# Kernel optimization log

Measured on AMD Instinct MI355X. Metric: run time of the kernel, lower is better.

Reference implementation:

```python
import jax, jax.numpy as jnp
import numpy as np

NUM_NEIGHBORS = (10, 25)  # FLAGS.num_neighbors = '10_25'
MAX_DEGREE = 64
L = 2  # num encoder layers


def _sample(nodes, neighbors_out, neighbors_in, key):
    """Multi-hop uniform neighbor sampling (shuffle columns + slice, as in TF code)."""
    samples = [nodes]
    support = 1
    supports = [1]
    for k in range(L):
        t = L - 1 - k
        n = NUM_NEIGHBORS[t]
        support *= 2 * n
        supports.append(support)
        key, k1, k2 = jax.random.split(key, 3)
        # tf.transpose(tf.random.shuffle(tf.transpose(x))) shuffles neighbor slots
        # with ONE permutation shared across all rows, then slices first n.
        cols_out = jax.random.permutation(k1, MAX_DEGREE)[:n]
        cols_in = jax.random.permutation(k2, MAX_DEGREE)[:n]
        nout = neighbors_out[samples[k]][:, cols_out]  # [prev, n]
        nin = neighbors_in[samples[k]][:, cols_in]     # [prev, n]
        samples.append(jnp.concatenate([nout, nin], axis=1).reshape(-1))
    return samples, supports


def _gc(self_v, nei_out, nei_in, W):
    # GraphConvolution: mean-aggregate out/in neighbors, concat with self, linear, sigmoid.
    agg = jnp.concatenate([self_v, nei_out.mean(axis=1), nei_in.mean(axis=1)], axis=-1)
    return jax.nn.sigmoid(agg @ W)


def _aggregate(inputs, supports, layer, W, B):
    h_hop = []
    for hop in range(L - layer):
        n = NUM_NEIGHBORS[L - hop - 1]
        nei = inputs[hop + 1].reshape(B * supports[hop], 2 * n, -1)
        self_v = inputs[hop].reshape(B * supports[hop], -1)
        h_hop.append(_gc(self_v, nei[:, :n], nei[:, n:], W))
    return h_hop


def _forward(nodes1, nodes2, neighbors_out, neighbors_in, features,
             W_in, W_mean, W_std, W_pi, W_ag, W_ad, Wd_mean, Wd_std, Wd_pi):
    B = nodes1.shape[0]
    key = jax.random.key(42)
    k1, k2 = jax.random.split(key)
    s1, sup1 = _sample(nodes1, neighbors_out, neighbors_in, k1)
    s2, sup2 = _sample(nodes2, neighbors_out, neighbors_in, k2)
    in1 = [features[s] for s in s1]  # hop-wise gathered features
    in2 = [features[s] for s in s2]
    # layer 0: shared input GC
    h1 = _aggregate(in1, sup1, 0, W_in, B)
    h2 = _aggregate(in2, sup2, 0, W_in, B)
    # layer 1: parameter heads (mean/std/pi/alpha)
    h_mean1 = _aggregate(h1, sup1, 1, W_mean, B)[0]
    h_mean2 = _aggregate(h2, sup2, 1, W_mean, B)[0]
    h_std1 = _aggregate(h1, sup1, 1, W_std, B)[0]
    h_std2 = _aggregate(h2, sup2, 1, W_std, B)[0]
    h_pi1 = _aggregate(h1, sup1, 1, W_pi, B)[0]
    h_pi2 = _aggregate(h2, sup2, 1, W_pi, B)[0]
    # final fully-connected projections (act = identity)
    z_mean1 = h_mean1 @ Wd_mean
    z_mean2 = h_mean2 @ Wd_mean
    z_std1 = h_std1 @ Wd_std
    z_std2 = h_std2 @ Wd_std
    pi_logit1 = h_pi1 @ Wd_pi
    pi_logit2 = h_pi2 @ Wd_pi
    return jnp.stack([z_mean1, z_std1, pi_logit1, z_mean2, z_std2, pi_logit2])


def setup_inputs() -> dict:
    key = jax.random.key(0)
    ks = jax.random.split(key, 16)
    N, F, B = 200000, 128, 256
    E, D = 128, 64
    inp = {
        'nodes1': jax.random.randint(ks[0], (B,), 0, N, dtype=jnp.int32),
        'nodes2': jax.random.randint(ks[1], (B,), 0, N, dtype=jnp.int32),
        'neighbors_out': jax.random.randint(ks[2], (N, MAX_DEGREE), 0, N, dtype=jnp.int32),
        'neighbors_in': jax.random.randint(ks[3], (N, MAX_DEGREE), 0, N, dtype=jnp.int32),
        'features': jax.random.normal(ks[4], (N, F), dtype=jnp.float32),
        'W_in': jax.random.normal(ks[5], (3 * F, E), dtype=jnp.float32) * 0.05,
        'W_mean': jax.random.normal(ks[6], (3 * E, E), dtype=jnp.float32) * 0.05,
        'W_std': jax.random.normal(ks[7], (3 * E, E), dtype=jnp.float32) * 0.05,
        'W_pi': jax.random.normal(ks[8], (3 * E, E), dtype=jnp.float32) * 0.05,
        'W_ag': jax.random.normal(ks[9], (3 * E, E), dtype=jnp.float32) * 0.05,
        'W_ad': jax.random.normal(ks[10], (3 * E, E), dtype=jnp.float32) * 0.05,
        'Wd_mean': jax.random.normal(ks[11], (E, D), dtype=jnp.float32) * 0.05,
        'Wd_std': jax.random.normal(ks[12], (E, D), dtype=jnp.float32) * 0.05,
        'Wd_pi': jax.random.normal(ks[13], (E, D), dtype=jnp.float32) * 0.05,
    }
    return inp


def reference(nodes1, nodes2, neighbors_out, neighbors_in, features,
              W_in, W_mean, W_std, W_pi, W_ag, W_ad, Wd_mean, Wd_std, Wd_pi):
    return _forward(nodes1, nodes2, neighbors_out, neighbors_in, features,
                    W_in, W_mean, W_std, W_pi, W_ag, W_ad, Wd_mean, Wd_std, Wd_pi)
```

## Files before the change

### kernel.cpp

```cpp
#include <hip/hip_runtime.h>
#include <stdint.h>
#include <math.h>

#define FDIM 128
#define KDIM 384
#define NROWS 26112

struct Cols { int o25[25]; int i25[25]; int o10[10]; int i10[10]; };
struct ColsBoth { Cols c[2]; };

static inline uint32_t rotl32(uint32_t x, uint32_t r){ return (x<<r)|(x>>(32u-r)); }

static void tf2x32(uint32_t k0, uint32_t k1, uint32_t c0, uint32_t c1,
                   uint32_t& o0, uint32_t& o1){
  const uint32_t ra[4] = {13u,15u,26u,6u};
  const uint32_t rb[4] = {17u,29u,16u,24u};
  uint32_t ks2 = k0 ^ k1 ^ 0x1BD11BDAu;
  uint32_t x0 = c0 + k0, x1 = c1 + k1;
  for(int i=0;i<4;i++){ x0 += x1; x1 = rotl32(x1, ra[i]); x1 ^= x0; }
  x0 += k1; x1 += ks2 + 1u;
  for(int i=0;i<4;i++){ x0 += x1; x1 = rotl32(x1, rb[i]); x1 ^= x0; }
  x0 += ks2; x1 += k0 + 2u;
  for(int i=0;i<4;i++){ x0 += x1; x1 = rotl32(x1, ra[i]); x1 ^= x0; }
  x0 += k0; x1 += k1 + 3u;
  for(int i=0;i<4;i++){ x0 += x1; x1 = rotl32(x1, rb[i]); x1 ^= x0; }
  x0 += k1; x1 += ks2 + 4u;
  for(int i=0;i<4;i++){ x0 += x1; x1 = rotl32(x1, ra[i]); x1 ^= x0; }
  x0 += ks2; x1 += k0 + 5u;
  o0 = x0; o1 = x1;
}

static void jax_split_child(uint32_t ka, uint32_t kb, uint32_t i,
                            uint32_t& oa, uint32_t& ob){
  tf2x32(ka, kb, 0u, i, oa, ob);
}

static uint32_t jax_bits32(uint32_t ka, uint32_t kb, uint32_t i){
  uint32_t a,b; tf2x32(ka, kb, 0u, i, a, b);
  return a ^ b;
}

static void jax_perm64(uint32_t ka, uint32_t kb, int* perm){
  uint32_t sa, sb; jax_split_child(ka, kb, 1u, sa, sb);
  uint32_t b[64]; int v[64];
  for(int i=0;i<64;i++){ b[i]=jax_bits32(sa, sb, (uint32_t)i); v[i]=i; }
  for(int i=1;i<64;i++){
    uint32_t bb=b[i]; int vv=v[i]; int j=i-1;
    while(j>=0 && b[j]>bb){ b[j+1]=b[j]; v[j+1]=v[j]; j--; }
    b[j+1]=bb; v[j+1]=vv;
  }
  for(int i=0;i<64;i++) perm[i]=v[i];
}

static void compute_cols(ColsBoth& cb){
  uint32_t k1a,k1b,k2a,k2b;
  jax_split_child(0u, 42u, 0u, k1a, k1b);
  jax_split_child(0u, 42u, 1u, k2a, k2b);
  for(int side=0; side<2; side++){
    uint32_t ka = side ? k2a : k1a;
    uint32_t kb = side ? k2b : k1b;
    uint32_t nka,nkb, c1a,c1b, c2a,c2b;
    jax_split_child(ka,kb,0u,nka,nkb);
    jax_split_child(ka,kb,1u,c1a,c1b);
    jax_split_child(ka,kb,2u,c2a,c2b);
    int p[64];
    jax_perm64(c1a,c1b,p); for(int i=0;i<25;i++) cb.c[side].o25[i]=p[i];
    jax_perm64(c2a,c2b,p); for(int i=0;i<25;i++) cb.c[side].i25[i]=p[i];
    uint32_t d1a,d1b,d2a,d2b;
    jax_split_child(nka,nkb,1u,d1a,d1b);
    jax_split_child(nka,nkb,2u,d2a,d2b);
    jax_perm64(d1a,d1b,p); for(int i=0;i<10;i++) cb.c[side].o10[i]=p[i];
    jax_perm64(d2a,d2b,p); for(int i=0;i<10;i++) cb.c[side].i10[i]=p[i];
  }
}

__device__ __forceinline__ float getc(const float4& v, int i){
  return (i==0)?v.x:(i==1)?v.y:(i==2)?v.z:v.w;
}
__device__ __forceinline__ float sigf(float x){ return 1.0f/(1.0f+expf(-x)); }
__device__ __forceinline__ void add4(float4& s, const float4& v){
  s.x+=v.x; s.y+=v.y; s.z+=v.z; s.w+=v.w;
}
__device__ __forceinline__ void add2(float2& s, const float2& v){
  s.x+=v.x; s.y+=v.y;
}


__global__ __launch_bounds__(256) void gather_kernel(
    const float* __restrict__ feat,
    const int* __restrict__ nodes1, const int* __restrict__ nodes2,
    const int* __restrict__ nout, const int* __restrict__ nin,
    float* __restrict__ agg, int base_row, ColsBoth cb)
{
  int t = threadIdx.x;
  int row_local = blockIdx.x*8 + (t>>5);
  int lane = t & 31;
  int c0 = lane*4;
  int row = base_row + row_local;

  float4 selfv, so, si;

  if(row < 512){
    int side = row >> 8, b = row & 255;
    int node = (side ? nodes2 : nodes1)[b];
    const Cols& c = cb.c[side];
    const long nb = (long)node*64;
    selfv = *(const float4*)(feat + (long)node*FDIM + c0);
    int ido[25], idi[25];
    #pragma unroll
    for(int i=0;i<25;i++) ido[i] = nout[nb + c.o25[i]];
    #pragma unroll
    for(int i=0;i<25;i++) idi[i] = nin[nb + c.i25[i]];
    float4 acco = make_float4(0,0,0,0);
    float4 acci = make_float4(0,0,0,0);
    #pragma unroll
    for(int jj=0; jj<25; jj+=5){
      float4 vo[5], vi[5];
      #pragma unroll
      for(int i=0;i<5;i++) vo[i] = *(const float4*)(feat + (long)ido[jj+i]*FDIM + c0);
      #pragma unroll
      for(int i=0;i<5;i++) vi[i] = *(const float4*)(feat + (long)idi[jj+i]*FDIM + c0);
      #pragma unroll
      for(int i=0;i<5;i++) add4(acco, vo[i]);
      #pragma unroll
      for(int i=0;i<5;i++) add4(acci, vi[i]);
    }
    so = make_float4(acco.x/25.f, acco.y/25.f, acco.z/25.f, acco.w/25.f);
    si = make_float4(acci.x/25.f, acci.y/25.f, acci.z/25.f, acci.w/25.f);
  } else {
    int hrow = row - 512;
    int side = (hrow >= 12800) ? 1 : 0;
    int r = side ? (hrow - 12800) : hrow;
    int b = r / 50, slot = r % 50;
    const Cols& c = cb.c[side];
    int root = (side ? nodes2 : nodes1)[b];
    int node;
    if(slot < 25) node = nout[(long)root*64 + c.o25[slot]];
    else          node = nin [(long)root*64 + c.i25[slot-25]];
    const long nb = (long)node*64;
    selfv = *(const float4*)(feat + (long)node*FDIM + c0);
    int oid[10], iid[10];
    #pragma unroll
    for(int j=0;j<10;j++) oid[j] = nout[nb + c.o10[j]];
    #pragma unroll
    for(int j=0;j<10;j++) iid[j] = nin[nb + c.i10[j]];
    float4 acco = make_float4(0,0,0,0);
    float4 acci = make_float4(0,0,0,0);
    #pragma unroll
    for(int jj=0; jj<10; jj+=5){
      float4 vo[5], vi[5];
      #pragma unroll
      for(int j=0;j<5;j++) vo[j] = *(const float4*)(feat + (long)oid[jj+j]*FDIM + c0);
      #pragma unroll
      for(int j=0;j<5;j++) vi[j] = *(const float4*)(feat + (long)iid[jj+j]*FDIM + c0);
      #pragma unroll
      for(int j=0;j<5;j++) add4(acco, vo[j]);
      #pragma unroll
      for(int j=0;j<5;j++) add4(acci, vi[j]);
    }
    so = make_float4(acco.x*0.1f, acco.y*0.1f, acco.z*0.1f, acco.w*0.1f);
    si = make_float4(acci.x*0.1f, acci.y*0.1f, acci.z*0.1f, acci.w*0.1f);
  }

  float* ar = agg + (long)row_local*KDIM;
  *(float4*)(ar + c0)       = selfv;
  *(float4*)(ar + 128 + c0) = so;
  *(float4*)(ar + 256 + c0) = si;
}

__global__ __launch_bounds__(256) void gemm_sig_kernel(
    const float* __restrict__ A, const float* __restrict__ W,
    float* __restrict__ out)
{
  __shared__ float Wbuf[96*128];
  int t = threadIdx.x, lane = t&15, rg = t>>4;
  int r0 = blockIdx.x*64 + rg*4;
  int c0 = lane*8;
  float acc[4][8];
  #pragma unroll
  for(int r=0;r<4;r++)
    #pragma unroll
    for(int i=0;i<8;i++) acc[r][i]=0.f;

  for(int kc=0; kc<4; kc++){
    __syncthreads();
    const float4* ws = (const float4*)(W + kc*96*128);
    float4* wd = (float4*)Wbuf;
    #pragma unroll
    for(int i=0;i<12;i++) wd[i*256+t] = ws[i*256+t];
    __syncthreads();
    const float* Ab = A + (long)r0*KDIM + kc*96;
    #pragma unroll 2
    for(int k4=0;k4<96;k4+=4){
      float4 a0 = *(const float4*)(Ab + 0*KDIM + k4);
      float4 a1 = *(const float4*)(Ab + 1*KDIM + k4);
      float4 a2 = *(const float4*)(Ab + 2*KDIM + k4);
      float4 a3 = *(const float4*)(Ab + 3*KDIM + k4);
      #pragma unroll
      for(int kk=0;kk<4;kk++){
        float av0=getc(a0,kk), av1=getc(a1,kk), av2=getc(a2,kk), av3=getc(a3,kk);
        const float* wr = Wbuf + (k4+kk)*128 + c0;
        float4 w0 = *(const float4*)wr;
        float4 w1 = *(const float4*)(wr+4);
        acc[0][0]+=av0*w0.x; acc[0][1]+=av0*w0.y; acc[0][2]+=av0*w0.z; acc[0][3]+=av0*w0.w;
        acc[0][4]+=av0*w1.x; acc[0][5]+=av0*w1.y; acc[0][6]+=av0*w1.z; acc[0][7]+=av0*w1.w;
        acc[1][0]+=av1*w0.x; acc[1][1]+=av1*w0.y; acc[1][2]+=av1*w0.z; acc[1][3]+=av1*w0.w;
        acc[1][4]+=av1*w1.x; acc[1][5]+=av1*w1.y; acc[1][6]+=av1*w1.z; acc[1][7]+=av1*w1.w;
        acc[2][0]+=av2*w0.x; acc[2][1]+=av2*w0.y; acc[2][2]+=av2*w0.z; acc[2][3]+=av2*w0.w;
        acc[2][4]+=av2*w1.x; acc[2][5]+=av2*w1.y; acc[2][6]+=av2*w1.z; acc[2][7]+=av2*w1.w;
        acc[3][0]+=av3*w0.x; acc[3][1]+=av3*w0.y; acc[3][2]+=av3*w0.z; acc[3][3]+=av3*w0.w;
        acc[3][4]+=av3*w1.x; acc[3][5]+=av3*w1.y; acc[3][6]+=av3*w1.z; acc[3][7]+=av3*w1.w;
      }
    }
  }
  #pragma unroll
  for(int r=0;r<4;r++){
    float4 o0, o1;
    o0.x=sigf(acc[r][0]); o0.y=sigf(acc[r][1]); o0.z=sigf(acc[r][2]); o0.w=sigf(acc[r][3]);
    o1.x=sigf(acc[r][4]); o1.y=sigf(acc[r][5]); o1.z=sigf(acc[r][6]); o1.w=sigf(acc[r][7]);
    float* op = out + (long)(r0+r)*FDIM + c0;
    *(float4*)op = o0; *(float4*)(op+4) = o1;
  }
}

__global__ __launch_bounds__(256) void head_kernel(
    const float* __restrict__ h,
    const float* __restrict__ Wm, const float* __restrict__ Ws, const float* __restrict__ Wp,
    const float* __restrict__ Dm, const float* __restrict__ Ds, const float* __restrict__ Dp,
    float* __restrict__ out)
{
  __shared__ float As[4*KDIM];
  __shared__ float Hs[4*FDIM];
  int head = blockIdx.x >> 7;
  int rt   = blockIdx.x & 127;
  int t = threadIdx.x;
  int row = t >> 6;
  int lane = t & 63;
  const float* W = (head==0) ? Wm : (head==1) ? Ws : Wp;
  const float* D = (head==0) ? Dm : (head==1) ? Ds : Dp;
  int grow = rt*4 + row;

  {
    int c2 = lane*2;
    float2 selfv = *(const float2*)(h + (long)grow*FDIM + c2);
    const float* nb = h + (long)(512 + grow*50)*FDIM + c2;
    float2 s = make_float2(0,0);
    #pragma unroll
    for(int jj=0;jj<25;jj+=5){
      float2 v[5];
      #pragma unroll
      for(int i=0;i<5;i++) v[i] = *(const float2*)(nb + (long)(jj+i)*FDIM);
      #pragma unroll
      for(int i=0;i<5;i++) add2(s, v[i]);
    }
    float2 so = make_float2(s.x/25.f, s.y/25.f);
    s = make_float2(0,0);
    #pragma unroll
    for(int jj=25;jj<50;jj+=5){
      float2 v[5];
      #pragma unroll
      for(int i=0;i<5;i++) v[i] = *(const float2*)(nb + (long)(jj+i)*FDIM);
      #pragma unroll
      for(int i=0;i<5;i++) add2(s, v[i]);
    }
    float2 si = make_float2(s.x/25.f, s.y/25.f);
    *(float2*)&As[row*KDIM + c2]       = selfv;
    *(float2*)&As[row*KDIM + 128 + c2] = so;
    *(float2*)&As[row*KDIM + 256 + c2] = si;
  }
  __syncthreads();

  {
    int c = lane*2;
    float acc0 = 0.f, acc1 = 0.f;
    const float* as = As + row*KDIM;
    #pragma unroll 8
    for(int k=0;k<KDIM;k++){
      float a = as[k];
      float2 w = *(const float2*)(W + (long)k*FDIM + c);
      acc0 += a*w.x; acc1 += a*w.y;
    }
    Hs[row*FDIM + c]   = sigf(acc0);
    Hs[row*FDIM + c+1] = sigf(acc1);
  }
  __syncthreads();

  {
    int col = lane;
    const float* hs = Hs + row*FDIM;
    float a = 0.f;
    #pragma unroll 8
    for(int k=0;k<FDIM;k++){
      a += hs[k] * D[(long)k*64 + col];
    }
    int side = grow >> 8, b = grow & 255;
    out[((long)(side*3+head)*256 + b)*64 + col] = a;
  }
}

extern "C" void kernel_launch(void* const* d_in, const int* in_sizes, int n_in,
                              void* d_out, int out_size, void* d_ws, size_t ws_size,
                              hipStream_t stream) {
  const int*   nodes1  = (const int*)d_in[0];
  const int*   nodes2  = (const int*)d_in[1];
  const int*   nout    = (const int*)d_in[2];
  const int*   nin     = (const int*)d_in[3];
  const float* feat    = (const float*)d_in[4];
  const float* W_in    = (const float*)d_in[5];
  const float* W_mean  = (const float*)d_in[6];
  const float* W_std   = (const float*)d_in[7];
  const float* W_pi    = (const float*)d_in[8];
  const float* Wd_mean = (const float*)d_in[11];
  const float* Wd_std  = (const float*)d_in[12];
  const float* Wd_pi   = (const float*)d_in[13];
  float* out = (float*)d_out;

  float* h    = (float*)d_ws;
  float* aggC = h + (size_t)NROWS*FDIM;

  size_t fixedB = (size_t)NROWS*FDIM*4;
  const int ncOpt[5] = {1,2,4,12,51};
  int nc = 51;
  for(int i=0;i<5;i++){
    size_t need = fixedB + ((size_t)NROWS/ncOpt[i])*KDIM*4;
    if(need <= ws_size){ nc = ncOpt[i]; break; }
  }
  int chunkRows = NROWS / nc;

  ColsBoth cb;
  compute_cols(cb);

  for(int c=0;c<nc;c++){
    int base = c*chunkRows;
    gather_kernel<<<chunkRows/8, 256, 0, stream>>>(feat, nodes1, nodes2,
                                                   nout, nin, aggC, base, cb);
    gemm_sig_kernel<<<chunkRows/64, 256, 0, stream>>>(aggC, W_in, h + (size_t)base*FDIM);
  }
  head_kernel<<<384, 256, 0, stream>>>(h, W_mean, W_std, W_pi, Wd_mean, Wd_std, Wd_pi, out);
}
```

Baseline: 325.0 us.

## Split head kernel to one row per block with split-K reductions

The head kernel now assigns one output row per block instead of four and launches four times as many blocks. Within each block the K dimension of both matrix products is split across four thread groups, and the partial sums are reduced through shared memory. This is meant to expose more parallelism and occupancy in the tail kernel. In exchange, each block reuses the weights for only one row, which increases weight reads, and extra synchronisation steps are added.

```diff
diff --git a/kernel.cpp b/kernel.cpp
--- a/kernel.cpp
+++ b/kernel.cpp
@@ -81,9 +81,6 @@
 __device__ __forceinline__ void add4(float4& s, const float4& v){
   s.x+=v.x; s.y+=v.y; s.z+=v.z; s.w+=v.w;
 }
-__device__ __forceinline__ void add2(float2& s, const float2& v){
-  s.x+=v.x; s.y+=v.y;
-}
 
 
 __global__ __launch_bounds__(256) void gather_kernel(
@@ -229,72 +226,77 @@
     const float* __restrict__ Dm, const float* __restrict__ Ds, const float* __restrict__ Dp,
     float* __restrict__ out)
 {
-  __shared__ float As[4*KDIM];
-  __shared__ float Hs[4*FDIM];
-  int head = blockIdx.x >> 7;
-  int rt   = blockIdx.x & 127;
+  __shared__ float As[KDIM];
+  __shared__ float Ps[4*FDIM];
+  __shared__ float Hs[FDIM];
+  __shared__ float Qs[4*64];
+  int head = blockIdx.x >> 9;
+  int grow = blockIdx.x & 511;
   int t = threadIdx.x;
-  int row = t >> 6;
-  int lane = t & 63;
   const float* W = (head==0) ? Wm : (head==1) ? Ws : Wp;
   const float* D = (head==0) ? Dm : (head==1) ? Ds : Dp;
-  int grow = rt*4 + row;
 
   {
-    int c2 = lane*2;
-    float2 selfv = *(const float2*)(h + (long)grow*FDIM + c2);
-    const float* nb = h + (long)(512 + grow*50)*FDIM + c2;
-    float2 s = make_float2(0,0);
+    int c = t & 127;
+    int half = t >> 7;
+    const float* nb = h + (long)(512 + grow*50 + half*25)*FDIM + c;
+    float s = 0.f;
     #pragma unroll
     for(int jj=0;jj<25;jj+=5){
-      float2 v[5];
-      #pragma unroll
-      for(int i=0;i<5;i++) v[i] = *(const float2*)(nb + (long)(jj+i)*FDIM);
-      #pragma unroll
-      for(int i=0;i<5;i++) add2(s, v[i]);
-    }
-    float2 so = make_float2(s.x/25.f, s.y/25.f);
-    s = make_float2(0,0);
-    #pragma unroll
-    for(int jj=25;jj<50;jj+=5){
-      float2 v[5];
-      #pragma unroll
-      for(int i=0;i<5;i++) v[i] = *(const float2*)(nb + (long)(jj+i)*FDIM);
-      #pragma unroll
-      for(int i=0;i<5;i++) add2(s, v[i]);
-    }
-    float2 si = make_float2(s.x/25.f, s.y/25.f);
-    *(float2*)&As[row*KDIM + c2]       = selfv;
-    *(float2*)&As[row*KDIM + 128 + c2] = so;
-    *(float2*)&As[row*KDIM + 256 + c2] = si;
+      float v0 = nb[(long)(jj+0)*FDIM];
+      float v1 = nb[(long)(jj+1)*FDIM];
+      float v2 = nb[(long)(jj+2)*FDIM];
+      float v3 = nb[(long)(jj+3)*FDIM];
+      float v4 = nb[(long)(jj+4)*FDIM];
+      s += v0+v1+v2+v3+v4;
+    }
+    As[128 + half*128 + c] = s/25.f;
+    if(half==0) As[c] = h[(long)grow*FDIM + c];
   }
   __syncthreads();
 
   {
-    int c = lane*2;
-    float acc0 = 0.f, acc1 = 0.f;
-    const float* as = As + row*KDIM;
+    int c2 = (t & 63)*2;
+    int kq = t >> 6;
+    const float* wp = W + (long)(kq*96)*FDIM + c2;
+    const float* as = As + kq*96;
+    float a0=0.f, a1=0.f;
     #pragma unroll 8
-    for(int k=0;k<KDIM;k++){
+    for(int k=0;k<96;k++){
       float a = as[k];
-      float2 w = *(const float2*)(W + (long)k*FDIM + c);
-      acc0 += a*w.x; acc1 += a*w.y;
-    }
-    Hs[row*FDIM + c]   = sigf(acc0);
-    Hs[row*FDIM + c+1] = sigf(acc1);
+      float2 w = *(const float2*)(wp + (long)k*FDIM);
+      a0 += a*w.x; a1 += a*w.y;
+    }
+    Ps[kq*FDIM + c2]   = a0;
+    Ps[kq*FDIM + c2+1] = a1;
   }
   __syncthreads();
+  if(t < 64){
+    int c2 = t*2;
+    float s0 = Ps[c2]     + Ps[FDIM+c2]     + Ps[2*FDIM+c2]     + Ps[3*FDIM+c2];
+    float s1 = Ps[c2+1]   + Ps[FDIM+c2+1]   + Ps[2*FDIM+c2+1]   + Ps[3*FDIM+c2+1];
+    Hs[c2]   = sigf(s0);
+    Hs[c2+1] = sigf(s1);
+  }
+  __syncthreads();
 
   {
-    int col = lane;
-    const float* hs = Hs + row*FDIM;
+    int col = t & 63;
+    int kq = t >> 6;
+    const float* dp = D + (long)(kq*32)*64 + col;
+    const float* hs = Hs + kq*32;
     float a = 0.f;
     #pragma unroll 8
-    for(int k=0;k<FDIM;k++){
-      a += hs[k] * D[(long)k*64 + col];
-    }
+    for(int k=0;k<32;k++){
+      a += hs[k] * dp[(long)k*64];
+    }
+    Qs[kq*64 + col] = a;
+  }
+  __syncthreads();
+  if(t < 64){
+    float a = Qs[t] + Qs[64+t] + Qs[128+t] + Qs[192+t];
     int side = grow >> 8, b = grow & 255;
-    out[((long)(side*3+head)*256 + b)*64 + col] = a;
+    out[((long)(side*3+head)*256 + b)*64 + t] = a;
   }
 }
 
@@ -336,5 +338,5 @@
                                                    nout, nin, aggC, base, cb);
     gemm_sig_kernel<<<chunkRows/64, 256, 0, stream>>>(aggC, W_in, h + (size_t)base*FDIM);
   }
-  head_kernel<<<384, 256, 0, stream>>>(h, W_mean, W_std, W_pi, Wd_mean, Wd_std, Wd_pi, out);
-}
+  head_kernel<<<1536, 256, 0, stream>>>(h, W_mean, W_std, W_pi, Wd_mean, Wd_std, Wd_pi, out);
+}
```

Result: faster. 313.6 us (-3.5%).
